# Kernel tuning notes

Hardware: AMD Instinct MI355X
Metric: run time of the kernel (lower is better)

The kernel has to match this reference:

```python
import jax, jax.numpy as jnp
import numpy as np

N, E, IN_DIM, HID, LAYERS = 300000, 600000, 64, 128, 2
BN_EPS = 1e-5

def setup_inputs() -> dict:
    key = jax.random.key(0)
    ks = jax.random.split(key, 8)
    scale_in = 1.0 / np.sqrt(IN_DIM)
    scale_h = 1.0 / np.sqrt(HID)
    return {
        "node_init": jax.random.normal(ks[0], (N, IN_DIM), dtype=jnp.float32),
        "edge_index": jax.random.randint(ks[1], (2, E), 0, N, dtype=jnp.int64),
        "edge_len": jax.random.uniform(ks[2], (E,), dtype=jnp.float32),
        "W_in": jax.random.normal(ks[3], (IN_DIM, HID), dtype=jnp.float32) * scale_in,
        "b_in": jnp.zeros((HID,), dtype=jnp.float32),
        "att_k": jax.random.normal(ks[4], (HID,), dtype=jnp.float32),
        "Wl": jax.random.normal(ks[5], (LAYERS, HID, HID), dtype=jnp.float32) * scale_h,
        "bl": jnp.zeros((LAYERS, HID), dtype=jnp.float32),
        "gamma": jnp.ones((LAYERS, HID), dtype=jnp.float32),
        "beta": jnp.zeros((LAYERS, HID), dtype=jnp.float32),
    }

def reference(node_init, edge_index, edge_len, W_in, b_in, att_k, Wl, bl, gamma, beta):
    src, dst = edge_index[0], edge_index[1]
    inv_len = 1.0 / (1.0 + edge_len)                     # [E]
    inv_sqrt_h = 1.0 / jnp.sqrt(jnp.asarray(HID, node_init.dtype))
    h = node_init @ W_in + b_in                          # [N,H]
    n = h.shape[0]
    for l in range(LAYERS):
        h_src = h[src]                                   # [E,H] gather
        key = (h_src @ att_k) * inv_sqrt_h               # [E]
        w = jnp.exp(key) * inv_len                       # [E]
        agg = jax.ops.segment_sum(w[:, None] * h_src, dst, num_segments=n)  # [N,H]
        h = h + jax.nn.relu(agg) @ Wl[l] + bl[l]
        mean = jnp.mean(h, axis=0)
        var = jnp.mean((h - mean) ** 2, axis=0)          # biased var (BatchNorm training)
        h = (h - mean) * jax.lax.rsqrt(var + BN_EPS) * gamma[l] + beta[l]
    return h
```

## Files before the change

kernel.cpp:

```cpp
#include <hip/hip_runtime.h>
#include <hip/hip_bf16.h>

#define N_NODES 300000
#define N_EDGES 600000
#define IN_DIMC 64
#define HIDC    128
#define NLAYERS 2
#define BN_EPS  1e-5f
#define INV_SQRT_H 0.08838834764831845f
#define NB_SCAN ((N_NODES + 255) / 256)
#define NTILES  (N_NODES / 16)

typedef __bf16 bf16x8 __attribute__((ext_vector_type(8)));
typedef float floatx4 __attribute__((ext_vector_type(4)));

__device__ int   g_row_ptr[N_NODES + 1];
__device__ int   g_cursor[N_NODES];
__device__ int   g_esrc[N_EDGES];
__device__ float g_einv[N_EDGES];
__device__ int   g_bsum[NB_SCAN];
__device__ __align__(16) __hip_bfloat16 g_Win_hi[128 * 64];
__device__ __align__(16) __hip_bfloat16 g_Win_lo[128 * 64];
__device__ __align__(16) __hip_bfloat16 g_Wl_hi[NLAYERS * 128 * 128];
__device__ __align__(16) __hip_bfloat16 g_Wl_lo[NLAYERS * 128 * 128];
__device__ float g_stats[NLAYERS * 2 * HIDC];
__device__ __align__(16) float g_bn_sc[NLAYERS * HIDC];
__device__ __align__(16) float g_bn_sh[NLAYERS * HIDC];

__device__ inline void split2(float x, __hip_bfloat16& hi, __hip_bfloat16& lo) {
    hi = __float2bfloat16(x);
    lo = __float2bfloat16(x - __bfloat162float(hi));
}

__global__ void zero_kernel() {
    int i = blockIdx.x * 256 + threadIdx.x;
    if (i < N_NODES) g_cursor[i] = 0;
    if (i < NLAYERS * 2 * HIDC) g_stats[i] = 0.f;
}

__global__ void prep_w_kernel(const float* __restrict__ W_in,
                              const float* __restrict__ Wl)
{
    int id = blockIdx.x * 256 + threadIdx.x;
    if (id < 128 * 64) {
        int n = id >> 6, k = id & 63;
        split2(W_in[k * 128 + n], g_Win_hi[id], g_Win_lo[id]);
    }
    if (id < NLAYERS * 128 * 128) {
        int l = id >> 14, r = id & 16383;
        int n = r >> 7, k = r & 127;
        split2(Wl[l * 16384 + k * 128 + n], g_Wl_hi[id], g_Wl_lo[id]);
    }
}

__global__ void hist_kernel(const int* __restrict__ dst)
{
    int e = blockIdx.x * 256 + threadIdx.x;
    if (e < N_EDGES) atomicAdd(&g_cursor[dst[e]], 1);
}

__global__ void scan1_kernel()
{
    __shared__ int tmp[256];
    int t = threadIdx.x;
    int i = blockIdx.x * 256 + t;
    tmp[t] = (i < N_NODES) ? g_cursor[i] : 0;
    __syncthreads();
    for (int d = 128; d > 0; d >>= 1) {
        if (t < d) tmp[t] += tmp[t + d];
        __syncthreads();
    }
    if (t == 0) g_bsum[blockIdx.x] = tmp[0];
}

__global__ void scan2_kernel()
{
    __shared__ int tmp[256];
    __shared__ int carry;
    int t = threadIdx.x;
    if (t == 0) { carry = 0; g_row_ptr[N_NODES] = N_EDGES; }
    __syncthreads();
    for (int base = 0; base < NB_SCAN; base += 256) {
        int i = base + t;
        int v = (i < NB_SCAN) ? g_bsum[i] : 0;
        tmp[t] = v;
        __syncthreads();
        for (int d = 1; d < 256; d <<= 1) {
            int x = (t >= d) ? tmp[t - d] : 0;
            __syncthreads();
            tmp[t] += x;
            __syncthreads();
        }
        int c = carry;
        if (i < NB_SCAN) g_bsum[i] = c + tmp[t] - v;
        __syncthreads();
        if (t == 0) carry = c + tmp[255];
        __syncthreads();
    }
}

__global__ void scan3_kernel()
{
    __shared__ int tmp[256];
    int t = threadIdx.x;
    int i = blockIdx.x * 256 + t;
    int v = (i < N_NODES) ? g_cursor[i] : 0;
    tmp[t] = v;
    __syncthreads();
    for (int d = 1; d < 256; d <<= 1) {
        int x = (t >= d) ? tmp[t - d] : 0;
        __syncthreads();
        tmp[t] += x;
        __syncthreads();
    }
    int r = g_bsum[blockIdx.x] + tmp[t] - v;
    if (i < N_NODES) { g_row_ptr[i] = r; g_cursor[i] = r; }
}

__global__ void scatter_kernel(const int* __restrict__ src, const int* __restrict__ dst,
                               const float* __restrict__ elen)
{
    int e = blockIdx.x * 256 + threadIdx.x;
    if (e >= N_EDGES) return;
    int d = dst[e];
    int pos = atomicAdd(&g_cursor[d], 1);
    g_esrc[pos] = src[e];
    g_einv[pos] = 1.0f / (1.0f + elen[e]);
}

__global__ __launch_bounds__(256) void edge_csr_kernel(
    const float* __restrict__ h, const float* __restrict__ att_k,
    float* __restrict__ agg, int prev)
{
    int lane = threadIdx.x & 63;
    int n = blockIdx.x * 4 + (threadIdx.x >> 6);
    if (n >= N_NODES) return;
    float2 ak = ((const float2*)att_k)[lane];
    float2 sc = make_float2(1.f, 1.f), sh = make_float2(0.f, 0.f);
    if (prev >= 0) {
        sc = ((const float2*)(g_bn_sc + prev * HIDC))[lane];
        sh = ((const float2*)(g_bn_sh + prev * HIDC))[lane];
    }
    int beg = g_row_ptr[n], end = g_row_ptr[n + 1];
    float a0 = 0.f, a1 = 0.f;
    for (int j = beg; j < end; ++j) {
        int s = g_esrc[j];
        float2 x = ((const float2*)(h + (size_t)s * HIDC))[lane];
        x.x = sc.x * x.x + sh.x;
        x.y = sc.y * x.y + sh.y;
        float p = x.x * ak.x + x.y * ak.y;
#pragma unroll
        for (int off = 32; off > 0; off >>= 1) p += __shfl_xor(p, off);
        float w = __expf(p * INV_SQRT_H) * g_einv[j];
        a0 += w * x.x;
        a1 += w * x.y;
    }
    float2 o;
    o.x = fmaxf(a0, 0.f);
    o.y = fmaxf(a1, 0.f);
    ((float2*)(agg + (size_t)n * HIDC))[lane] = o;
}

__global__ __launch_bounds__(256) void proj_mfma_kernel(
    const float* __restrict__ X, const float* __restrict__ b,
    float* __restrict__ h)
{
    __shared__ __align__(16) __hip_bfloat16 Ah[64 * 72];
    __shared__ __align__(16) __hip_bfloat16 Al[64 * 72];
    __shared__ __align__(16) __hip_bfloat16 Bh[128 * 72];
    __shared__ __align__(16) __hip_bfloat16 Bl[128 * 72];
    int t = threadIdx.x;
    int nbase = blockIdx.x * 64;

    for (int i = t; i < 1024; i += 256) {
        int row = i >> 3, c8 = i & 7;
        *(float4*)((char*)Bh + row * 144 + c8 * 16) =
            *(const float4*)((const char*)g_Win_hi + row * 128 + c8 * 16);
        *(float4*)((char*)Bl + row * 144 + c8 * 16) =
            *(const float4*)((const char*)g_Win_lo + row * 128 + c8 * 16);
    }
    for (int i = t; i < 1024; i += 256) {
        int row = i >> 4, c4 = i & 15;
        int n = nbase + row;
        float4 v = make_float4(0.f, 0.f, 0.f, 0.f);
        if (n < N_NODES) v = *(const float4*)(X + (size_t)n * IN_DIMC + c4 * 4);
        union { __hip_bfloat16 e[4]; uint2 u; } ph, pl;
        split2(v.x, ph.e[0], pl.e[0]); split2(v.y, ph.e[1], pl.e[1]);
        split2(v.z, ph.e[2], pl.e[2]); split2(v.w, ph.e[3], pl.e[3]);
        *(uint2*)((char*)Ah + row * 144 + c4 * 8) = ph.u;
        *(uint2*)((char*)Al + row * 144 + c4 * 8) = pl.u;
    }
    __syncthreads();

    int lane = t & 63, w = t >> 6;
    int m16 = lane & 15, quad = lane >> 4;
    floatx4 acc[8];
#pragma unroll
    for (int i = 0; i < 8; ++i) acc[i] = floatx4{0.f, 0.f, 0.f, 0.f};

#pragma unroll
    for (int kk = 0; kk < 64; kk += 32) {
        bf16x8 ah = *(const bf16x8*)((const char*)Ah + (w * 16 + m16) * 144 + (kk + quad * 8) * 2);
        bf16x8 al = *(const bf16x8*)((const char*)Al + (w * 16 + m16) * 144 + (kk + quad * 8) * 2);
#pragma unroll
        for (int nt = 0; nt < 8; ++nt) {
            bf16x8 bh = *(const bf16x8*)((const char*)Bh + (nt * 16 + m16) * 144 + (kk + quad * 8) * 2);
            bf16x8 bl = *(const bf16x8*)((const char*)Bl + (nt * 16 + m16) * 144 + (kk + quad * 8) * 2);
            acc[nt] = __builtin_amdgcn_mfma_f32_16x16x32_bf16(ah, bh, acc[nt], 0, 0, 0);
            acc[nt] = __builtin_amdgcn_mfma_f32_16x16x32_bf16(al, bh, acc[nt], 0, 0, 0);
            acc[nt] = __builtin_amdgcn_mfma_f32_16x16x32_bf16(ah, bl, acc[nt], 0, 0, 0);
        }
    }
#pragma unroll
    for (int nt = 0; nt < 8; ++nt) {
        int ch = nt * 16 + m16;
        float bias = b[ch];
#pragma unroll
        for (int r = 0; r < 4; ++r) {
            int n = nbase + w * 16 + quad * 4 + r;
            if (n < N_NODES) h[(size_t)n * HIDC + ch] = acc[nt][r] + bias;
        }
    }
}

__global__ __launch_bounds__(256) void layer_gemm_kernel(
    float* __restrict__ h, const float* __restrict__ agg,
    const float* __restrict__ b, int layer, int prev)
{
    __shared__ __align__(16) __hip_bfloat16 Bh[128 * 136];
    __shared__ __align__(16) __hip_bfloat16 Bl[128 * 136];
    __shared__ float red[256];
    int t = threadIdx.x;
    const __hip_bfloat16* Wh = g_Wl_hi + layer * 16384;
    const __hip_bfloat16* Wlo = g_Wl_lo + layer * 16384;
    red[t] = 0.f;

    for (int i = t; i < 2048; i += 256) {
        int row = i >> 4, c8 = i & 15;
        *(float4*)((char*)Bh + row * 272 + c8 * 16) =
            *(const float4*)((const char*)Wh + row * 256 + c8 * 16);
        *(float4*)((char*)Bl + row * 272 + c8 * 16) =
            *(const float4*)((const char*)Wlo + row * 256 + c8 * 16);
    }
    __syncthreads();

    const int lane = t & 63, w = t >> 6;
    const int m16 = lane & 15, quad = lane >> 4;
    const int wid = blockIdx.x * 4 + w;
    const int nwaves = gridDim.x * 4;

    float bias[8], scp[8], shp[8];
#pragma unroll
    for (int nt = 0; nt < 8; ++nt) {
        int ch = nt * 16 + m16;
        bias[nt] = b[ch];
        scp[nt] = (prev >= 0) ? g_bn_sc[prev * HIDC + ch] : 1.f;
        shp[nt] = (prev >= 0) ? g_bn_sh[prev * HIDC + ch] : 0.f;
    }
    float sreg[8], qreg[8];
#pragma unroll
    for (int nt = 0; nt < 8; ++nt) { sreg[nt] = 0.f; qreg[nt] = 0.f; }

    for (int tile = wid; tile < NTILES; tile += nwaves) {
        const float* arow = agg + (size_t)(tile * 16 + m16) * HIDC + quad * 8;
        floatx4 acc[8];
#pragma unroll
        for (int i = 0; i < 8; ++i) acc[i] = floatx4{0.f, 0.f, 0.f, 0.f};

#pragma unroll
        for (int kk = 0; kk < 4; ++kk) {
            float4 a0 = *(const float4*)(arow + kk * 32);
            float4 a1 = *(const float4*)(arow + kk * 32 + 4);
            union { __hip_bfloat16 e[8]; bf16x8 v; } ah, al;
            split2(a0.x, ah.e[0], al.e[0]); split2(a0.y, ah.e[1], al.e[1]);
            split2(a0.z, ah.e[2], al.e[2]); split2(a0.w, ah.e[3], al.e[3]);
            split2(a1.x, ah.e[4], al.e[4]); split2(a1.y, ah.e[5], al.e[5]);
            split2(a1.z, ah.e[6], al.e[6]); split2(a1.w, ah.e[7], al.e[7]);
#pragma unroll
            for (int nt = 0; nt < 8; ++nt) {
                const char* bp = (const char*)Bh + (nt * 16 + m16) * 272 + (kk * 32 + quad * 8) * 2;
                const char* lp = (const char*)Bl + (nt * 16 + m16) * 272 + (kk * 32 + quad * 8) * 2;
                bf16x8 bh = *(const bf16x8*)bp;
                bf16x8 bl = *(const bf16x8*)lp;
                acc[nt] = __builtin_amdgcn_mfma_f32_16x16x32_bf16(ah.v, bh, acc[nt], 0, 0, 0);
                acc[nt] = __builtin_amdgcn_mfma_f32_16x16x32_bf16(al.v, bh, acc[nt], 0, 0, 0);
                acc[nt] = __builtin_amdgcn_mfma_f32_16x16x32_bf16(ah.v, bl, acc[nt], 0, 0, 0);
            }
        }
        int node0 = tile * 16 + quad * 4;
#pragma unroll
        for (int nt = 0; nt < 8; ++nt) {
            int ch = nt * 16 + m16;
#pragma unroll
            for (int r = 0; r < 4; ++r) {
                float* hp = h + (size_t)(node0 + r) * HIDC + ch;
                float o = scp[nt] * (*hp) + shp[nt] + acc[nt][r] + bias[nt];
                *hp = o;
                sreg[nt] += o;
                qreg[nt] += o * o;
            }
        }
    }

#pragma unroll
    for (int nt = 0; nt < 8; ++nt) {
        float s = sreg[nt], q = qreg[nt];
        s += __shfl_xor(s, 16); s += __shfl_xor(s, 32);
        q += __shfl_xor(q, 16); q += __shfl_xor(q, 32);
        if (quad == 0) {
            atomicAdd(&red[nt * 16 + m16], s);
            atomicAdd(&red[HIDC + nt * 16 + m16], q);
        }
    }
    __syncthreads();
    atomicAdd(&g_stats[layer * 2 * HIDC + t], red[t]);
}

__global__ void bn_prep_kernel(const float* __restrict__ gamma,
                               const float* __restrict__ beta, int layer)
{
    int c = threadIdx.x;
    if (c >= HIDC) return;
    const float invN = 1.0f / (float)N_NODES;
    float mean = g_stats[layer * 2 * HIDC + c] * invN;
    float var = g_stats[layer * 2 * HIDC + HIDC + c] * invN - mean * mean;
    float s = gamma[layer * HIDC + c] * rsqrtf(var + BN_EPS);
    g_bn_sc[layer * HIDC + c] = s;
    g_bn_sh[layer * HIDC + c] = beta[layer * HIDC + c] - mean * s;
}

__global__ __launch_bounds__(256) void bn_apply_kernel(float* __restrict__ h, int layer)
{
    size_t idx = (size_t)blockIdx.x * 256 + threadIdx.x;
    if (idx >= (size_t)N_NODES * (HIDC / 4)) return;
    int cg = (int)(idx & 31);
    float4 sc = ((const float4*)(g_bn_sc + layer * HIDC))[cg];
    float4 sh = ((const float4*)(g_bn_sh + layer * HIDC))[cg];
    float4 v = ((float4*)h)[idx];
    v.x = sc.x * v.x + sh.x;
    v.y = sc.y * v.y + sh.y;
    v.z = sc.z * v.z + sh.z;
    v.w = sc.w * v.w + sh.w;
    ((float4*)h)[idx] = v;
}

extern "C" void kernel_launch(void* const* d_in, const int* in_sizes, int n_in,
                              void* d_out, int out_size, void* d_ws, size_t ws_size,
                              hipStream_t stream) {
    (void)in_sizes; (void)n_in; (void)out_size; (void)ws_size;
    const float* node_init = (const float*)d_in[0];
    const int*   eidx      = (const int*)d_in[1];
    const float* elen      = (const float*)d_in[2];
    const float* W_in      = (const float*)d_in[3];
    const float* b_in      = (const float*)d_in[4];
    const float* att_k     = (const float*)d_in[5];
    const float* Wl        = (const float*)d_in[6];
    const float* bl        = (const float*)d_in[7];
    const float* gamma     = (const float*)d_in[8];
    const float* beta      = (const float*)d_in[9];

    float* h   = (float*)d_out;
    float* agg = (float*)d_ws;

    const int* src = eidx;
    const int* dst = eidx + N_EDGES;

    zero_kernel<<<NB_SCAN, 256, 0, stream>>>();
    hist_kernel<<<(N_EDGES + 255) / 256, 256, 0, stream>>>(dst);
    scan1_kernel<<<NB_SCAN, 256, 0, stream>>>();
    scan2_kernel<<<1, 256, 0, stream>>>();
    scan3_kernel<<<NB_SCAN, 256, 0, stream>>>();
    scatter_kernel<<<(N_EDGES + 255) / 256, 256, 0, stream>>>(src, dst, elen);
    prep_w_kernel<<<(NLAYERS * 128 * 128 + 255) / 256, 256, 0, stream>>>(W_in, Wl);

    proj_mfma_kernel<<<(N_NODES + 63) / 64, 256, 0, stream>>>(node_init, b_in, h);

    for (int l = 0; l < NLAYERS; ++l) {
        edge_csr_kernel<<<(N_NODES + 3) / 4, 256, 0, stream>>>(h, att_k, agg, l - 1);
        layer_gemm_kernel<<<512, 256, 0, stream>>>(h, agg, bl + (size_t)l * HIDC, l, l - 1);
        bn_prep_kernel<<<1, 128, 0, stream>>>(gamma, beta, l);
    }
    bn_apply_kernel<<<(N_NODES * (HIDC / 4) + 255) / 256, 256, 0, stream>>>(h, NLAYERS - 1);
}
```

Baseline: 958.4 us.

## Precompute per-node attention keys and hoist BN affine out of edge loop

The attention key depends only on the source node, so exp(key) is now computed once per node: fused into the input projection epilogue for the first layer, and done by a new key_kernel for later layers. The edge aggregation loop then reads one precomputed scalar per edge instead of doing a wave-wide shuffle reduction and exp. It also applies the previous layer's BN scale and shift once at the end, via the accumulated weight sum, and unrolls by two. Edge source and inverse length are packed into one int2 array. This removes redundant per-edge reductions in exchange for an extra pass over h per layer and a small extra node-sized buffer.

```diff
diff --git a/kernel.cpp b/kernel.cpp
--- a/kernel.cpp
+++ b/kernel.cpp
@@ -16,9 +16,9 @@
 
 __device__ int   g_row_ptr[N_NODES + 1];
 __device__ int   g_cursor[N_NODES];
-__device__ int   g_esrc[N_EDGES];
-__device__ float g_einv[N_EDGES];
+__device__ __align__(8) int2 g_edge[N_EDGES];
 __device__ int   g_bsum[NB_SCAN];
+__device__ float g_ekey[N_NODES];
 __device__ __align__(16) __hip_bfloat16 g_Win_hi[128 * 64];
 __device__ __align__(16) __hip_bfloat16 g_Win_lo[128 * 64];
 __device__ __align__(16) __hip_bfloat16 g_Wl_hi[NLAYERS * 128 * 128];
@@ -124,46 +124,55 @@
     if (e >= N_EDGES) return;
     int d = dst[e];
     int pos = atomicAdd(&g_cursor[d], 1);
-    g_esrc[pos] = src[e];
-    g_einv[pos] = 1.0f / (1.0f + elen[e]);
+    int2 ed;
+    ed.x = src[e];
+    ed.y = __float_as_int(1.0f / (1.0f + elen[e]));
+    g_edge[pos] = ed;
 }
 
 __global__ __launch_bounds__(256) void edge_csr_kernel(
-    const float* __restrict__ h, const float* __restrict__ att_k,
-    float* __restrict__ agg, int prev)
+    const float* __restrict__ h, float* __restrict__ agg, int prev)
 {
     int lane = threadIdx.x & 63;
     int n = blockIdx.x * 4 + (threadIdx.x >> 6);
     if (n >= N_NODES) return;
-    float2 ak = ((const float2*)att_k)[lane];
+    int beg = g_row_ptr[n], end = g_row_ptr[n + 1];
+    float a0 = 0.f, a1 = 0.f, sw = 0.f;
+    const float2* h2 = (const float2*)h;
+    int j = beg;
+    for (; j + 1 < end; j += 2) {
+        int2 e0 = g_edge[j];
+        int2 e1 = g_edge[j + 1];
+        float w0 = g_ekey[e0.x] * __int_as_float(e0.y);
+        float w1 = g_ekey[e1.x] * __int_as_float(e1.y);
+        float2 x0 = h2[(size_t)e0.x * 64 + lane];
+        float2 x1 = h2[(size_t)e1.x * 64 + lane];
+        a0 += w0 * x0.x + w1 * x1.x;
+        a1 += w0 * x0.y + w1 * x1.y;
+        sw += w0 + w1;
+    }
+    if (j < end) {
+        int2 e0 = g_edge[j];
+        float w0 = g_ekey[e0.x] * __int_as_float(e0.y);
+        float2 x0 = h2[(size_t)e0.x * 64 + lane];
+        a0 += w0 * x0.x;
+        a1 += w0 * x0.y;
+        sw += w0;
+    }
     float2 sc = make_float2(1.f, 1.f), sh = make_float2(0.f, 0.f);
     if (prev >= 0) {
         sc = ((const float2*)(g_bn_sc + prev * HIDC))[lane];
         sh = ((const float2*)(g_bn_sh + prev * HIDC))[lane];
     }
-    int beg = g_row_ptr[n], end = g_row_ptr[n + 1];
-    float a0 = 0.f, a1 = 0.f;
-    for (int j = beg; j < end; ++j) {
-        int s = g_esrc[j];
-        float2 x = ((const float2*)(h + (size_t)s * HIDC))[lane];
-        x.x = sc.x * x.x + sh.x;
-        x.y = sc.y * x.y + sh.y;
-        float p = x.x * ak.x + x.y * ak.y;
-#pragma unroll
-        for (int off = 32; off > 0; off >>= 1) p += __shfl_xor(p, off);
-        float w = __expf(p * INV_SQRT_H) * g_einv[j];
-        a0 += w * x.x;
-        a1 += w * x.y;
-    }
     float2 o;
-    o.x = fmaxf(a0, 0.f);
-    o.y = fmaxf(a1, 0.f);
+    o.x = fmaxf(sc.x * a0 + sh.x * sw, 0.f);
+    o.y = fmaxf(sc.y * a1 + sh.y * sw, 0.f);
     ((float2*)(agg + (size_t)n * HIDC))[lane] = o;
 }
 
 __global__ __launch_bounds__(256) void proj_mfma_kernel(
     const float* __restrict__ X, const float* __restrict__ b,
-    float* __restrict__ h)
+    const float* __restrict__ att_k, float* __restrict__ h)
 {
     __shared__ __align__(16) __hip_bfloat16 Ah[64 * 72];
     __shared__ __align__(16) __hip_bfloat16 Al[64 * 72];
@@ -211,16 +220,49 @@
             acc[nt] = __builtin_amdgcn_mfma_f32_16x16x32_bf16(ah, bl, acc[nt], 0, 0, 0);
         }
     }
+    float dotr[4] = {0.f, 0.f, 0.f, 0.f};
 #pragma unroll
     for (int nt = 0; nt < 8; ++nt) {
         int ch = nt * 16 + m16;
         float bias = b[ch];
+        float ak = att_k[ch];
 #pragma unroll
         for (int r = 0; r < 4; ++r) {
             int n = nbase + w * 16 + quad * 4 + r;
-            if (n < N_NODES) h[(size_t)n * HIDC + ch] = acc[nt][r] + bias;
-        }
-    }
+            float o = acc[nt][r] + bias;
+            if (n < N_NODES) h[(size_t)n * HIDC + ch] = o;
+            dotr[r] += ak * o;
+        }
+    }
+#pragma unroll
+    for (int r = 0; r < 4; ++r) {
+        float p = dotr[r];
+        p += __shfl_xor(p, 1); p += __shfl_xor(p, 2);
+        p += __shfl_xor(p, 4); p += __shfl_xor(p, 8);
+        int n = nbase + w * 16 + quad * 4 + r;
+        if (m16 == 0 && n < N_NODES) g_ekey[n] = __expf(p * INV_SQRT_H);
+    }
+}
+
+__global__ __launch_bounds__(256) void key_kernel(const float* __restrict__ h,
+                                                  const float* __restrict__ att_k,
+                                                  int prev)
+{
+    int t = threadIdx.x;
+    int lane = t & 63;
+    int half = lane >> 5, sub = lane & 31;
+    int n = (blockIdx.x * 4 + (t >> 6)) * 2 + half;
+    if (n >= N_NODES) return;
+    float4 x = ((const float4*)h)[(size_t)n * 32 + sub];
+    float4 sc = ((const float4*)(g_bn_sc + prev * HIDC))[sub];
+    float4 sh = ((const float4*)(g_bn_sh + prev * HIDC))[sub];
+    float4 ak = ((const float4*)att_k)[sub];
+    float p = (sc.x * x.x + sh.x) * ak.x + (sc.y * x.y + sh.y) * ak.y +
+              (sc.z * x.z + sh.z) * ak.z + (sc.w * x.w + sh.w) * ak.w;
+    p += __shfl_xor(p, 1);  p += __shfl_xor(p, 2);
+    p += __shfl_xor(p, 4);  p += __shfl_xor(p, 8);
+    p += __shfl_xor(p, 16);
+    if (sub == 0) g_ekey[n] = __expf(p * INV_SQRT_H);
 }
 
 __global__ __launch_bounds__(256) void layer_gemm_kernel(
@@ -278,10 +320,8 @@
             split2(a1.z, ah.e[6], al.e[6]); split2(a1.w, ah.e[7], al.e[7]);
 #pragma unroll
             for (int nt = 0; nt < 8; ++nt) {
-                const char* bp = (const char*)Bh + (nt * 16 + m16) * 272 + (kk * 32 + quad * 8) * 2;
-                const char* lp = (const char*)Bl + (nt * 16 + m16) * 272 + (kk * 32 + quad * 8) * 2;
-                bf16x8 bh = *(const bf16x8*)bp;
-                bf16x8 bl = *(const bf16x8*)lp;
+                bf16x8 bh = *(const bf16x8*)((const char*)Bh + (nt * 16 + m16) * 272 + (kk * 32 + quad * 8) * 2);
+                bf16x8 bl = *(const bf16x8*)((const char*)Bl + (nt * 16 + m16) * 272 + (kk * 32 + quad * 8) * 2);
                 acc[nt] = __builtin_amdgcn_mfma_f32_16x16x32_bf16(ah.v, bh, acc[nt], 0, 0, 0);
                 acc[nt] = __builtin_amdgcn_mfma_f32_16x16x32_bf16(al.v, bh, acc[nt], 0, 0, 0);
                 acc[nt] = __builtin_amdgcn_mfma_f32_16x16x32_bf16(ah.v, bl, acc[nt], 0, 0, 0);
@@ -373,10 +413,12 @@
     scatter_kernel<<<(N_EDGES + 255) / 256, 256, 0, stream>>>(src, dst, elen);
     prep_w_kernel<<<(NLAYERS * 128 * 128 + 255) / 256, 256, 0, stream>>>(W_in, Wl);
 
-    proj_mfma_kernel<<<(N_NODES + 63) / 64, 256, 0, stream>>>(node_init, b_in, h);
+    proj_mfma_kernel<<<(N_NODES + 63) / 64, 256, 0, stream>>>(node_init, b_in, att_k, h);
 
     for (int l = 0; l < NLAYERS; ++l) {
-        edge_csr_kernel<<<(N_NODES + 3) / 4, 256, 0, stream>>>(h, att_k, agg, l - 1);
+        if (l > 0)
+            key_kernel<<<(N_NODES / 2 + 3) / 4, 256, 0, stream>>>(h, att_k, l - 1);
+        edge_csr_kernel<<<(N_NODES + 3) / 4, 256, 0, stream>>>(h, agg, l - 1);
         layer_gemm_kernel<<<512, 256, 0, stream>>>(h, agg, bl + (size_t)l * HIDC, l, l - 1);
         bn_prep_kernel<<<1, 128, 0, stream>>>(gamma, beta, l);
     }
```

Measured after the change: 942.4 us. Within noise of the previous version (-1.7%).
